# Optimization experiments

Hardware: AMD Instinct MI355X
Metric: run time of the kernel (lower is better)

The kernel has to match this reference:

```python
import jax, jax.numpy as jnp
import numpy as np

B, L, H = 4, 1024, 1024
NH, HD = 16, 64
ND = NH * HD
ITERS = 4
U = 5  # MSA1 ring window size (hard-coded in source)


def _conv1x1(w, b, x):  # w [O,C], b [O], x [B,C,L] -> [B,O,L]  (Conv2d 1x1 == per-position linear)
    return jnp.einsum('oc,bcl->bol', w, x) + b[None, :, None]


def _layernorm(x, s, b, eps=1e-5):  # x [B,H,L]; LayerNorm over channel dim H
    mu = x.mean(1, keepdims=True)
    var = ((x - mu) ** 2).mean(1, keepdims=True)
    return (x - mu) / jnp.sqrt(var + eps) * s[None, :, None] + b[None, :, None]


def _msa1(x, ax, wq, bq, wk, bk, wv, bv, wo, bo):
    # x [B,H,L] normalized nodes; ax [B,H,2,L] (ring embedding + relay)
    b, h, l = x.shape
    q = _conv1x1(wq, bq, x).reshape(b, NH, HD, l)
    k = _conv1x1(wk, bk, x).reshape(b, NH, HD, l)
    v = _conv1x1(wv, bv, x).reshape(b, NH, HD, l)
    pad = U // 2
    kp = jnp.pad(k, ((0, 0), (0, 0), (0, 0), (pad, pad)))
    vp = jnp.pad(v, ((0, 0), (0, 0), (0, 0), (pad, pad)))
    # F.unfold with (U,1) kernel along L == stack of U shifted views
    kw = jnp.stack([kp[..., u:u + l] for u in range(U)], axis=3)  # [B,NH,HD,U,L]
    vw = jnp.stack([vp[..., u:u + l] for u in range(U)], axis=3)
    al = ax.shape[2]
    ak = (jnp.einsum('oc,bcal->boal', wk, ax) + bk[None, :, None, None]).reshape(b, NH, HD, al, l)
    av = (jnp.einsum('oc,bcal->boal', wv, ax) + bv[None, :, None, None]).reshape(b, NH, HD, al, l)
    kw = jnp.concatenate([kw, ak], axis=3)  # [B,NH,HD,U+2,L]
    vw = jnp.concatenate([vw, av], axis=3)
    scores = (q[:, :, :, None, :] * kw).sum(2) / np.sqrt(HD)  # [B,NH,U+2,L]
    alphas = jax.nn.softmax(scores, axis=2)
    att = (alphas[:, :, None, :, :] * vw).sum(3).reshape(b, ND, l)
    return _conv1x1(wo, bo, att)  # [B,H,L]


def _msa2(relay, y, smask, wq, bq, wk, bk, wo, bo):
    # relay [B,H]; y [B,H,L+1]; smask [B,L+1] True at padding
    b = relay.shape[0]
    q = (jnp.einsum('oc,bc->bo', wq, relay) + bq).reshape(b, NH, HD)
    k = _conv1x1(wk, bk, y).reshape(b, NH, HD, -1)
    pre = jnp.einsum('bnd,bndl->bnl', q, k) / np.sqrt(HD)
    pre = jnp.where(smask[:, None, :], -1e10, pre)
    alphas = jax.nn.softmax(pre, axis=-1)
    # NOTE: source has v = k (WV output unused) -- reproduced faithfully
    att = jnp.einsum('bnl,bndl->bnd', alphas, k).reshape(b, ND)
    return jnp.einsum('oc,bc->bo', wo, att) + bo  # [B,H]


def _star_forward(data, mask, ln_s, ln_b, rwq, rwq_b, rwk, rwk_b, rwv, rwv_b, rwo, rwo_b,
                  swq, swq_b, swk, swk_b, swo, swo_b):
    b, l, h = data.shape
    pad_mask = (mask == 0)  # True at padding positions
    smask = jnp.concatenate([jnp.zeros((b, 1), bool), pad_mask], axis=1)  # [B,L+1]
    embs = jnp.transpose(data, (0, 2, 1))  # [B,H,L]
    nodes = embs
    relay = embs.mean(2)  # [B,H]
    for i in range(ITERS):
        xn = _layernorm(nodes, ln_s[i], ln_b[i])
        ax = jnp.stack([embs, jnp.broadcast_to(relay[:, :, None], embs.shape)], axis=2)  # [B,H,2,L]
        ring = _msa1(xn, ax, rwq[i], rwq_b[i], rwk[i], rwk_b[i], rwv[i], rwv_b[i], rwo[i], rwo_b[i])
        nodes = nodes + jax.nn.leaky_relu(ring)
        y = jnp.concatenate([relay[:, :, None], nodes], axis=2)  # [B,H,L+1]
        relay = jax.nn.leaky_relu(_msa2(relay, y, smask, swq[i], swq_b[i], swk[i], swk_b[i], swo[i], swo_b[i]))
        nodes = jnp.where(pad_mask[:, None, :], 0.0, nodes)
    return jnp.transpose(nodes, (0, 2, 1)), relay  # [B,L,H], [B,H]


def setup_inputs() -> dict:
    key = jax.random.key(0)
    ks = jax.random.split(key, 16)
    def p(k, shape):
        return jax.random.normal(k, shape, jnp.float32) * 0.02
    return dict(
        data=jax.random.normal(ks[0], (B, L, H), jnp.float32),
        mask=jax.random.randint(ks[1], (B, L), 0, 2).astype(jnp.int32),
        ln_s=jnp.ones((ITERS, H), jnp.float32),
        ln_b=jnp.zeros((ITERS, H), jnp.float32),
        rwq=p(ks[2], (ITERS, ND, H)), rwq_b=p(ks[3], (ITERS, ND)),
        rwk=p(ks[4], (ITERS, ND, H)), rwk_b=p(ks[5], (ITERS, ND)),
        rwv=p(ks[6], (ITERS, ND, H)), rwv_b=p(ks[7], (ITERS, ND)),
        rwo=p(ks[8], (ITERS, H, ND)), rwo_b=p(ks[9], (ITERS, H)),
        swq=p(ks[10], (ITERS, ND, H)), swq_b=p(ks[11], (ITERS, ND)),
        swk=p(ks[12], (ITERS, ND, H)), swk_b=p(ks[13], (ITERS, ND)),
        swo=p(ks[14], (ITERS, H, ND)), swo_b=p(ks[15], (ITERS, H)),
    )


def reference(data, mask, ln_s, ln_b, rwq, rwq_b, rwk, rwk_b, rwv, rwv_b, rwo, rwo_b,
              swq, swq_b, swk, swk_b, swo, swo_b):
    return _star_forward(data, mask, ln_s, ln_b, rwq, rwq_b, rwk, rwk_b, rwv, rwv_b,
                         rwo, rwo_b, swq, swq_b, swk, swk_b, swo, swo_b)
```

## Files before the change

kernel.cpp:

```cpp
#include <hip/hip_runtime.h>
#include <math.h>

namespace {

constexpr int B_ = 4, L_ = 1024, H_ = 1024, NH_ = 16, HD_ = 64, ND_ = 1024, ITERS_ = 4;

typedef unsigned short u16;
typedef __attribute__((ext_vector_type(8))) short short8;
typedef __attribute__((ext_vector_type(4))) float f32x4;

__device__ inline u16 f2bf(float f) {
  unsigned u = __builtin_bit_cast(unsigned, f);
  u += 0x7FFFu + ((u >> 16) & 1u);
  return (u16)(u >> 16);
}
__device__ inline float bf2f(u16 v) {
  unsigned u = ((unsigned)v) << 16;
  return __builtin_bit_cast(float, u);
}

__device__ inline void gl_lds16(const u16* g, u16* l) {
  __builtin_amdgcn_global_load_lds((const __attribute__((address_space(1))) void*)g,
                                   (__attribute__((address_space(3))) void*)l, 16, 0, 0);
}

__global__ void k_prep(const float* __restrict__ data, const float* __restrict__ rwq,
                       const float* __restrict__ rwk, const float* __restrict__ rwv,
                       const float* __restrict__ rwo, const float* __restrict__ swk,
                       u16* __restrict__ embs_bf, u16* __restrict__ wq_bf,
                       u16* __restrict__ wk_bf, u16* __restrict__ wv_bf,
                       u16* __restrict__ wo_bf, u16* __restrict__ swk_bf,
                       float* __restrict__ nodes) {
  int i = blockIdx.x * 256 + threadIdx.x;
  int which = blockIdx.y;
  if (which == 6) {
    reinterpret_cast<float4*>(nodes)[i] = reinterpret_cast<const float4*>(data)[i];
    return;
  }
  const float* src;
  u16* dst;
  switch (which) {
    case 0: src = data; dst = embs_bf; break;
    case 1: src = rwq; dst = wq_bf; break;
    case 2: src = rwk; dst = wk_bf; break;
    case 3: src = rwv; dst = wv_bf; break;
    case 4: src = rwo; dst = wo_bf; break;
    default: src = swk; dst = swk_bf; break;
  }
  float4 v = reinterpret_cast<const float4*>(src)[i];
  ushort4 o;
  o.x = f2bf(v.x); o.y = f2bf(v.y); o.z = f2bf(v.z); o.w = f2bf(v.w);
  reinterpret_cast<ushort4*>(dst)[i] = o;
}

__global__ void k_relay_part(const float* __restrict__ data, float* __restrict__ part) {
  int b = blockIdx.z, chunk = blockIdx.y;
  int c = blockIdx.x * 256 + threadIdx.x;
  const float* p = data + ((size_t)b * L_ + chunk * 128) * H_ + c;
  float acc = 0.f;
  for (int l = 0; l < 128; ++l) acc += p[(size_t)l * H_];
  part[((size_t)b * 8 + chunk) * H_ + c] = acc;
}
__global__ void k_relay_reduce(const float* __restrict__ part, float* __restrict__ relay) {
  int i = blockIdx.x * 256 + threadIdx.x;
  int b = i >> 10, c = i & 1023;
  float acc = 0.f;
  for (int j = 0; j < 8; ++j) acc += part[((size_t)b * 8 + j) * H_ + c];
  relay[i] = acc * (1.f / (float)L_);
}

__global__ __launch_bounds__(256) void k_layernorm_bf(float* __restrict__ nodes,
                                                      const float* __restrict__ s,
                                                      const float* __restrict__ bb,
                                                      const int* __restrict__ mask,
                                                      u16* __restrict__ y, int do_zero) {
  int row = blockIdx.x * 4 + (threadIdx.x >> 6);
  int lane = threadIdx.x & 63;
  int b = row >> 10, l = row & 1023;
  bool pad = do_zero && (mask[b * L_ + l] == 0);
  float4* xr = reinterpret_cast<float4*>(nodes + (size_t)row * H_);
  float4 v[4];
  float sum = 0.f, sq = 0.f;
#pragma unroll
  for (int j = 0; j < 4; ++j) {
    v[j] = pad ? float4{0.f, 0.f, 0.f, 0.f} : xr[lane + 64 * j];
    sum += v[j].x + v[j].y + v[j].z + v[j].w;
    sq += v[j].x * v[j].x + v[j].y * v[j].y + v[j].z * v[j].z + v[j].w * v[j].w;
  }
  if (pad) {
#pragma unroll
    for (int j = 0; j < 4; ++j) xr[lane + 64 * j] = float4{0.f, 0.f, 0.f, 0.f};
  }
#pragma unroll
  for (int off = 32; off; off >>= 1) {
    sum += __shfl_xor(sum, off);
    sq += __shfl_xor(sq, off);
  }
  float mu = sum * (1.f / (float)H_);
  float rstd = rsqrtf(sq * (1.f / (float)H_) - mu * mu + 1e-5f);
  ushort4* yr = reinterpret_cast<ushort4*>(y + (size_t)row * H_);
#pragma unroll
  for (int j = 0; j < 4; ++j) {
    int c4 = lane + 64 * j;
    float4 sc = reinterpret_cast<const float4*>(s)[c4];
    float4 bc = reinterpret_cast<const float4*>(bb)[c4];
    ushort4 o;
    o.x = f2bf((v[j].x - mu) * rstd * sc.x + bc.x);
    o.y = f2bf((v[j].y - mu) * rstd * sc.y + bc.y);
    o.z = f2bf((v[j].z - mu) * rstd * sc.z + bc.z);
    o.w = f2bf((v[j].w - mu) * rstd * sc.w + bc.w);
    yr[c4] = o;
  }
}


#define GEMM_PROLOGUE(XPTR, WPTR)                                              \
  __shared__ __align__(16) u16 sX[2][128 * 32];                                \
  __shared__ __align__(16) u16 sW[2][128 * 32];                                \
  const int t = threadIdx.x;                                                   \
  const int w = t >> 6, lane = t & 63;                                         \
  const int wm = w >> 1, wn = w & 1;                                           \
  const int r4 = lane >> 2, slot = lane & 3;                                   \
  const int rowS0 = w * 16 + r4, rowS1 = 64 + rowS0;                           \
  const int colS0 = ((slot ^ ((rowS0 >> 1) & 3)) << 3);                        \
  const int colS1 = ((slot ^ ((rowS1 >> 1) & 3)) << 3);                        \
  const u16* gX0 = (XPTR) + (size_t)(bm + rowS0) * 1024 + colS0;               \
  const u16* gX1 = (XPTR) + (size_t)(bm + rowS1) * 1024 + colS1;               \
  const u16* gW0 = (WPTR) + (size_t)(bn + rowS0) * 1024 + colS0;               \
  const u16* gW1 = (WPTR) + (size_t)(bn + rowS1) * 1024 + colS1;               \
  u16* lX0a = sX[0] + w * 512;                                                 \
  u16* lX0b = sX[1] + w * 512;                                                 \
  u16* lX1a = sX[0] + (4 + w) * 512;                                           \
  u16* lX1b = sX[1] + (4 + w) * 512;                                           \
  u16* lW0a = sW[0] + w * 512;                                                 \
  u16* lW0b = sW[1] + w * 512;                                                 \
  u16* lW1a = sW[0] + (4 + w) * 512;                                           \
  u16* lW1b = sW[1] + (4 + w) * 512;                                           \
  const int kidx = (((lane >> 4) ^ ((lane >> 1) & 3)) << 3);                   \
  f32x4 acc[4][4];                                                             \
  _Pragma("unroll") for (int i_ = 0; i_ < 4; ++i_)                             \
      _Pragma("unroll") for (int j_ = 0; j_ < 4; ++j_)                         \
          acc[i_][j_] = f32x4{0.f, 0.f, 0.f, 0.f};

#define GEMM_KLOOP64(AROWBASE, BROWBASE, ASRC, BSRC)                           \
  for (int ck = 0; ck < 1024; ck += 64) {                                      \
    gl_lds16(gX0, lX0a);                                                       \
    gl_lds16(gX0 + 32, lX0b);                                                  \
    gl_lds16(gX1, lX1a);                                                       \
    gl_lds16(gX1 + 32, lX1b);                                                  \
    gl_lds16(gW0, lW0a);                                                       \
    gl_lds16(gW0 + 32, lW0b);                                                  \
    gl_lds16(gW1, lW1a);                                                       \
    gl_lds16(gW1 + 32, lW1b);                                                  \
    gX0 += 64; gX1 += 64; gW0 += 64; gW1 += 64;                                \
    __syncthreads();                                                           \
    _Pragma("unroll") for (int h = 0; h < 2; ++h) {                            \
      short8 af_[4], bf_[4];                                                   \
      _Pragma("unroll") for (int mf = 0; mf < 4; ++mf)                         \
          af_[mf] = *reinterpret_cast<const short8*>(                          \
              &ASRC[h][((AROWBASE) + mf * 16) * 32 + kidx]);                   \
      _Pragma("unroll") for (int nf = 0; nf < 4; ++nf)                         \
          bf_[nf] = *reinterpret_cast<const short8*>(                          \
              &BSRC[h][((BROWBASE) + nf * 16) * 32 + kidx]);                   \
      _Pragma("unroll") for (int mf = 0; mf < 4; ++mf)                         \
          _Pragma("unroll") for (int nf = 0; nf < 4; ++nf)                     \
              acc[mf][nf] = __builtin_amdgcn_mfma_f32_16x16x32_bf16(           \
                  af_[mf], bf_[nf], acc[mf][nf], 0, 0, 0);                     \
    }                                                                          \
    __syncthreads();                                                          \
  }

__global__ __launch_bounds__(256, 3) void k_gemm5(const u16* __restrict__ wq,
                                                  const u16* __restrict__ wk,
                                                  const u16* __restrict__ wv,
                                                  const float* __restrict__ bq,
                                                  const float* __restrict__ bk,
                                                  const float* __restrict__ bv,
                                                  const u16* __restrict__ xn,
                                                  const u16* __restrict__ embs,
                                                  u16* __restrict__ Y) {
  const int orig = blockIdx.y * 32 + blockIdx.x;
  const int swz = (orig & 7) * 160 + (orig >> 3);
  const int sbx = swz & 31, sby = swz >> 5;
  const int bm = sbx * 128;
  const int which = sby >> 3;
  const int bn = (sby & 7) * 128;
  const u16* W = (which == 0) ? wq : ((which == 1 || which == 3) ? wk : wv);
  const float* bias = (which == 0) ? bq : ((which == 1 || which == 3) ? bk : bv);
  const u16* X = (which < 3) ? xn : embs;
  u16* Yw = Y + (size_t)which * ((size_t)B_ * L_ * ND_);

  GEMM_PROLOGUE(X, W)
  const int rW = wm * 64 + (lane & 15);
  const int rX = wn * 64 + (lane & 15);
  GEMM_KLOOP64(rW, rX, sW, sX)

#pragma unroll
  for (int mo = 0; mo < 4; ++mo) {
    int o0 = bn + wm * 64 + mo * 16 + ((lane >> 4) << 2);
    float4 bs = *reinterpret_cast<const float4*>(bias + o0);
#pragma unroll
    for (int nl = 0; nl < 4; ++nl) {
      int bl = bm + wn * 64 + nl * 16 + (lane & 15);
      f32x4 vv = acc[mo][nl];
      ushort4 ov;
      ov.x = f2bf(vv[0] + bs.x);
      ov.y = f2bf(vv[1] + bs.y);
      ov.z = f2bf(vv[2] + bs.z);
      ov.w = f2bf(vv[3] + bs.w);
      *reinterpret_cast<ushort4*>(&Yw[(size_t)bl * 1024 + o0]) = ov;
    }
  }
}

__global__ __launch_bounds__(256, 3) void k_gemm_wo(const u16* __restrict__ W,
                                                    const float* __restrict__ bias,
                                                    const u16* __restrict__ X,
                                                    float* __restrict__ nodes,
                                                    u16* __restrict__ nodes_bf) {
  const int orig = blockIdx.y * 32 + blockIdx.x;
  const int swz = (orig & 7) * 32 + (orig >> 3);
  const int bm = (swz & 31) * 128;
  const int bn = (swz >> 5) * 128;
  GEMM_PROLOGUE(X, W)
  const int rW = wm * 64 + (lane & 15);
  const int rX = wn * 64 + (lane & 15);
  GEMM_KLOOP64(rW, rX, sW, sX)

#pragma unroll
  for (int mo = 0; mo < 4; ++mo) {
    int o0 = bn + wm * 64 + mo * 16 + ((lane >> 4) << 2);
    float4 bs = *reinterpret_cast<const float4*>(bias + o0);
#pragma unroll
    for (int nl = 0; nl < 4; ++nl) {
      int bl = bm + wn * 64 + nl * 16 + (lane & 15);
      size_t ni = (size_t)bl * 1024 + o0;
      float4 curv = *reinterpret_cast<const float4*>(&nodes[ni]);
      f32x4 vv = acc[mo][nl];
      float r0 = vv[0] + bs.x; r0 = curv.x + (r0 > 0.f ? r0 : 0.01f * r0);
      float r1 = vv[1] + bs.y; r1 = curv.y + (r1 > 0.f ? r1 : 0.01f * r1);
      float r2 = vv[2] + bs.z; r2 = curv.z + (r2 > 0.f ? r2 : 0.01f * r2);
      float r3 = vv[3] + bs.w; r3 = curv.w + (r3 > 0.f ? r3 : 0.01f * r3);
      *reinterpret_cast<float4*>(&nodes[ni]) = float4{r0, r1, r2, r3};
      ushort4 ov;
      ov.x = f2bf(r0); ov.y = f2bf(r1); ov.z = f2bf(r2); ov.w = f2bf(r3);
      *reinterpret_cast<ushort4*>(&nodes_bf[ni]) = ov;
    }
  }
}

__global__ __launch_bounds__(256, 3) void k_gemm_kkb(const u16* __restrict__ W,
                                                     const float* __restrict__ bias,
                                                     const u16* __restrict__ X,
                                                     float* __restrict__ Y) {
  const int orig = blockIdx.y * 32 + blockIdx.x;
  const int swz = (orig & 7) * 32 + (orig >> 3);
  const int bm = (swz & 31) * 128;
  const int bn = (swz >> 5) * 128;
  GEMM_PROLOGUE(X, W)
  const int rX = wm * 64 + (lane & 15);
  const int rW = wn * 64 + (lane & 15);
  GEMM_KLOOP64(rX, rW, sX, sW)

#pragma unroll
  for (int nf = 0; nf < 4; ++nf) {
    int o = bn + wn * 64 + nf * 16 + (lane & 15);
    float bs = bias[o];
#pragma unroll
    for (int mf = 0; mf < 4; ++mf) {
      int gl = bm + wm * 64 + mf * 16 + ((lane >> 4) << 2);
      int b = gl >> 10, l = gl & 1023;
      size_t yi = ((size_t)(b * 1024 + o)) * (size_t)(L_ + 1) + 1 + l;
      f32x4 v = acc[mf][nf];
#pragma unroll
      for (int r = 0; r < 4; ++r) Y[yi + r] = v[r] + bs;
    }
  }
}

__global__ __launch_bounds__(256) void k_matvec2(const float* __restrict__ W0,
                                                 const float* __restrict__ b0,
                                                 float* __restrict__ y0, long sB0, long sO0,
                                                 const float* __restrict__ W1,
                                                 const float* __restrict__ b1,
                                                 float* __restrict__ y1, long sB1, long sO1,
                                                 const float* __restrict__ x) {
  int b = blockIdx.y;
  int z = blockIdx.z;
  const float* W = z ? W1 : W0;
  const float* bias = z ? b1 : b0;
  float* y = z ? y1 : y0;
  long sB = z ? sB1 : sB0, sO = z ? sO1 : sO0;
  int o = blockIdx.x * 4 + (threadIdx.x >> 6);
  int lane = threadIdx.x & 63;
  const float* wr = W + (size_t)o * 1024;
  const float* xb = x + (size_t)b * 1024;
  float acc = 0.f;
  for (int c = lane; c < 1024; c += 64) acc += wr[c] * xb[c];
#pragma unroll
  for (int off = 32; off; off >>= 1) acc += __shfl_xor(acc, off);
  if (lane == 0) y[(size_t)b * sB + (size_t)o * sO] = acc + bias[o];
}

__global__ __launch_bounds__(256) void k_matvec(const float* __restrict__ W,
                                                const float* __restrict__ bias,
                                                const float* __restrict__ x,
                                                float* __restrict__ y, int leaky) {
  int b = blockIdx.y;
  int o = blockIdx.x * 4 + (threadIdx.x >> 6);
  int lane = threadIdx.x & 63;
  const float* wr = W + (size_t)o * 1024;
  const float* xb = x + (size_t)b * 1024;
  float acc = 0.f;
  for (int c = lane; c < 1024; c += 64) acc += wr[c] * xb[c];
#pragma unroll
  for (int off = 32; off; off >>= 1) acc += __shfl_xor(acc, off);
  if (lane == 0) {
    acc += bias[o];
    if (leaky) acc = acc > 0.f ? acc : 0.01f * acc;
    y[(size_t)b * 1024 + o] = acc;
  }
}

__global__ __launch_bounds__(256) void k_msa1(const u16* __restrict__ q,
                                              const u16* __restrict__ k,
                                              const u16* __restrict__ v,
                                              const u16* __restrict__ ke,
                                              const u16* __restrict__ ve,
                                              const float* __restrict__ rk,
                                              const float* __restrict__ rv,
                                              u16* __restrict__ attbf) {
  int t = threadIdx.x;
  int wv = t >> 6, lane = t & 63;
  int head = lane >> 2, dq = lane & 3;
  int l = blockIdx.x * 4 + wv;
  int b = blockIdx.z;
  size_t row = ((size_t)(b * 1024 + l)) * 1024 + head * 64 + dq * 16;
  size_t rbase = (size_t)b * 1024 + head * 64 + dq * 16;

  float qf[16];
  {
    const short8* qp = reinterpret_cast<const short8*>(q + row);
#pragma unroll
    for (int j = 0; j < 2; ++j) {
      short8 qv = qp[j];
#pragma unroll
      for (int e = 0; e < 8; ++e) qf[j * 8 + e] = bf2f((u16)qv[e]);
    }
  }
  float s[7];
#pragma unroll
  for (int u = 0; u < 5; ++u) {
    int lk = l + u - 2;
    float su = 0.f;
    if (lk >= 0 && lk < L_) {
      const short8* kp = reinterpret_cast<const short8*>(
          k + ((size_t)(b * 1024 + lk)) * 1024 + head * 64 + dq * 16);
#pragma unroll
      for (int j = 0; j < 2; ++j) {
        short8 kv = kp[j];
#pragma unroll
        for (int e = 0; e < 8; ++e) su = fmaf(qf[j * 8 + e], bf2f((u16)kv[e]), su);
      }
    }
    s[u] = su;
  }
  {
    float su = 0.f;
    const short8* kp = reinterpret_cast<const short8*>(ke + row);
#pragma unroll
    for (int j = 0; j < 2; ++j) {
      short8 kv = kp[j];
#pragma unroll
      for (int e = 0; e < 8; ++e) su = fmaf(qf[j * 8 + e], bf2f((u16)kv[e]), su);
    }
    s[5] = su;
  }
  {
    float su = 0.f;
    const float4* rp = reinterpret_cast<const float4*>(rk + rbase);
#pragma unroll
    for (int j = 0; j < 4; ++j) {
      float4 r4 = rp[j];
      su = fmaf(qf[j * 4 + 0], r4.x, su);
      su = fmaf(qf[j * 4 + 1], r4.y, su);
      su = fmaf(qf[j * 4 + 2], r4.z, su);
      su = fmaf(qf[j * 4 + 3], r4.w, su);
    }
    s[6] = su;
  }
#pragma unroll
  for (int u = 0; u < 7; ++u) {
    s[u] += __shfl_xor(s[u], 1);
    s[u] += __shfl_xor(s[u], 2);
  }
  float m = -1e30f;
#pragma unroll
  for (int u = 0; u < 7; ++u) {
    s[u] *= 0.125f;
    m = fmaxf(m, s[u]);
  }
  float e[7], tot = 0.f;
#pragma unroll
  for (int u = 0; u < 7; ++u) {
    e[u] = expf(s[u] - m);
    tot += e[u];
  }
  float inv = 1.f / tot;
#pragma unroll
  for (int u = 0; u < 7; ++u) e[u] *= inv;

  float av[16];
  {
    const float4* rp = reinterpret_cast<const float4*>(rv + rbase);
#pragma unroll
    for (int j = 0; j < 4; ++j) {
      float4 r4 = rp[j];
      av[j * 4 + 0] = e[6] * r4.x;
      av[j * 4 + 1] = e[6] * r4.y;
      av[j * 4 + 2] = e[6] * r4.z;
      av[j * 4 + 3] = e[6] * r4.w;
    }
  }
  {
    const short8* vp = reinterpret_cast<const short8*>(ve + row);
#pragma unroll
    for (int j = 0; j < 2; ++j) {
      short8 vvv = vp[j];
#pragma unroll
      for (int ee = 0; ee < 8; ++ee) av[j * 8 + ee] = fmaf(e[5], bf2f((u16)vvv[ee]), av[j * 8 + ee]);
    }
  }
#pragma unroll
  for (int u = 0; u < 5; ++u) {
    int lk = l + u - 2;
    if (lk >= 0 && lk < L_) {
      const short8* vp = reinterpret_cast<const short8*>(
          v + ((size_t)(b * 1024 + lk)) * 1024 + head * 64 + dq * 16);
#pragma unroll
      for (int j = 0; j < 2; ++j) {
        short8 vvv = vp[j];
#pragma unroll
        for (int ee = 0; ee < 8; ++ee) av[j * 8 + ee] = fmaf(e[u], bf2f((u16)vvv[ee]), av[j * 8 + ee]);
      }
    }
  }
  u16 ob[16];
#pragma unroll
  for (int j = 0; j < 16; ++j) ob[j] = f2bf(av[j]);
  uint4* d4 = reinterpret_cast<uint4*>(attbf + row);
  const uint4* s4 = reinterpret_cast<const uint4*>(ob);
  d4[0] = s4[0];
  d4[1] = s4[1];
}

__global__ __launch_bounds__(256) void k_msa2p(const float* __restrict__ rq,
                                               const float* __restrict__ kk,
                                               const int* __restrict__ mask,
                                               float* __restrict__ pw,
                                               float* __restrict__ pE) {
  int n = blockIdx.x, c = blockIdx.y, b = blockIdx.z;
  int tid = threadIdx.x;
  __shared__ float sq_[HD_];
  __shared__ float se[260];
  size_t rb = (size_t)(b * NH_ + n) * HD_;
  if (tid < HD_) sq_[tid] = rq[rb + tid];
  __syncthreads();
  const float* kb = kk + rb * (size_t)(L_ + 1);
  int p0 = c * 256;
  {
    int p = p0 + tid;
    float e;
    if (p > 0 && mask[b * L_ + p - 1] == 0) {
      e = 0.f;
    } else {
      float acc = 0.f;
      for (int d = 0; d < HD_; ++d) acc = fmaf(sq_[d], kb[(size_t)d * (L_ + 1) + p], acc);
      e = expf(acc * 0.125f);
    }
    se[tid] = e;
  }
  int nP = 256;
  if (c == 3) {
    nP = 257;
    if (tid == 0) {
      float e;
      if (mask[b * L_ + 1023] == 0) {
        e = 0.f;
      } else {
        float acc = 0.f;
        for (int d = 0; d < HD_; ++d) acc = fmaf(sq_[d], kb[(size_t)d * (L_ + 1) + 1024], acc);
        e = expf(acc * 0.125f);
      }
      se[256] = e;
    }
  }
  __syncthreads();
  int lane = tid & 63, w = tid >> 6;
  if (w == 0) {
    float E = 0.f;
    for (int i = lane; i < nP; i += 64) E += se[i];
#pragma unroll
    for (int off = 32; off; off >>= 1) E += __shfl_xor(E, off);
    if (lane == 0) pE[((size_t)(b * NH_ + n)) * 4 + c] = E;
  }
  for (int dd = 0; dd < 16; ++dd) {
    int d = w * 16 + dd;
    const float* kd = kb + (size_t)d * (L_ + 1) + p0;
    float a = 0.f;
    for (int i = lane; i < nP; i += 64) a = fmaf(se[i], kd[i], a);
#pragma unroll
    for (int off = 32; off; off >>= 1) a += __shfl_xor(a, off);
    if (lane == 0) pw[(((size_t)(b * NH_ + n)) * 4 + c) * HD_ + d] = a;
  }
}

__global__ void k_msa2r(const float* __restrict__ pw, const float* __restrict__ pE,
                        float* __restrict__ satt) {
  int i = blockIdx.x * 256 + threadIdx.x;
  int bn = i >> 6, d = i & 63;
  float E = pE[bn * 4 + 0] + pE[bn * 4 + 1] + pE[bn * 4 + 2] + pE[bn * 4 + 3];
  float ws = pw[((size_t)bn * 4 + 0) * HD_ + d] + pw[((size_t)bn * 4 + 1) * HD_ + d] +
             pw[((size_t)bn * 4 + 2) * HD_ + d] + pw[((size_t)bn * 4 + 3) * HD_ + d];
  satt[i] = ws / E;
}

__global__ void k_final(const float* __restrict__ nodes, const int* __restrict__ mask,
                        float* __restrict__ out) {
  int i = blockIdx.x * 256 + threadIdx.x;
  int row = i >> 8;
  int b = row >> 10, l = row & 1023;
  float4 v = (mask[b * L_ + l] == 0) ? float4{0.f, 0.f, 0.f, 0.f}
                                     : reinterpret_cast<const float4*>(nodes)[i];
  reinterpret_cast<float4*>(out)[i] = v;
}

__global__ void k_copy_relay(const float* __restrict__ relay, float* __restrict__ out) {
  int i = blockIdx.x * 256 + threadIdx.x;
  out[i] = relay[i];
}

}

extern "C" void kernel_launch(void* const* d_in, const int* in_sizes, int n_in,
                              void* d_out, int out_size, void* d_ws, size_t ws_size,
                              hipStream_t stream) {
  (void)in_sizes; (void)n_in; (void)out_size; (void)ws_size;
  const float* data = (const float*)d_in[0];
  const int* mask = (const int*)d_in[1];
  const float* ln_s = (const float*)d_in[2];
  const float* ln_b = (const float*)d_in[3];
  const float* rwq = (const float*)d_in[4];
  const float* rwq_b = (const float*)d_in[5];
  const float* rwk = (const float*)d_in[6];
  const float* rwk_b = (const float*)d_in[7];
  const float* rwv = (const float*)d_in[8];
  const float* rwv_b = (const float*)d_in[9];
  const float* rwo = (const float*)d_in[10];
  const float* rwo_b = (const float*)d_in[11];
  const float* swq = (const float*)d_in[12];
  const float* swq_b = (const float*)d_in[13];
  const float* swk = (const float*)d_in[14];
  const float* swk_b = (const float*)d_in[15];
  const float* swo = (const float*)d_in[16];
  const float* swo_b = (const float*)d_in[17];
  float* out = (float*)d_out;

  const size_t SZ = (size_t)B_ * ND_ * L_;
  float* f = (float*)d_ws;
  float* nodes = f; f += SZ;
  float* kkb = f; f += (size_t)B_ * ND_ * (L_ + 1);
  float* part = f; f += (size_t)B_ * 8 * H_;
  float* relay = f; f += B_ * H_;
  float* rk = f; f += B_ * ND_;
  float* rv = f; f += B_ * ND_;
  float* rq = f; f += B_ * ND_;
  float* satt = f; f += B_ * ND_;
  float* pw = f; f += (size_t)B_ * NH_ * 4 * HD_;
  float* pE = f; f += B_ * NH_ * 4;
  u16* u = (u16*)f;
  u16* xn_bf = u; u += SZ;
  u16* embs_bf = u; u += SZ;
  u16* att_bf = u; u += SZ;
  u16* nodes_bf = u; u += SZ;
  u16* qkv5_bf = u; u += 5 * SZ;
  u16* wq_bf = u; u += SZ;
  u16* wk_bf = u; u += SZ;
  u16* wv_bf = u; u += SZ;
  u16* wo_bf = u; u += SZ;
  u16* swk_bf = u; u += SZ;

  k_prep<<<dim3(4096, 7), 256, 0, stream>>>(data, rwq, rwk, rwv, rwo, swk,
                                            embs_bf, wq_bf, wk_bf, wv_bf, wo_bf, swk_bf, nodes);
  k_relay_part<<<dim3(H_ / 256, 8, B_), 256, 0, stream>>>(data, part);
  k_relay_reduce<<<dim3((B_ * H_) / 256), 256, 0, stream>>>(part, relay);

  for (int i = 0; i < ITERS_; ++i) {
    const u16* wq_i = wq_bf + (size_t)i * ND_ * H_;
    const u16* wk_i = wk_bf + (size_t)i * ND_ * H_;
    const u16* wv_i = wv_bf + (size_t)i * ND_ * H_;
    const u16* wo_i = wo_bf + (size_t)i * H_ * ND_;
    const u16* sk_i = swk_bf + (size_t)i * ND_ * H_;

    k_layernorm_bf<<<dim3(B_ * L_ / 4), 256, 0, stream>>>(nodes, ln_s + i * H_, ln_b + i * H_,
                                                          mask, xn_bf, i > 0 ? 1 : 0);
    k_gemm5<<<dim3(32, 40), 256, 0, stream>>>(wq_i, wk_i, wv_i,
                                              rwq_b + i * ND_, rwk_b + i * ND_, rwv_b + i * ND_,
                                              xn_bf, embs_bf, qkv5_bf);
    k_matvec2<<<dim3(256, B_, 2), 256, 0, stream>>>(
        rwk + (size_t)i * ND_ * H_, rwk_b + i * ND_, rk, ND_, 1,
        rwv + (size_t)i * ND_ * H_, rwv_b + i * ND_, rv, ND_, 1, relay);
    k_msa1<<<dim3(L_ / 4, 1, B_), 256, 0, stream>>>(qkv5_bf, qkv5_bf + SZ, qkv5_bf + 2 * SZ,
                                                    qkv5_bf + 3 * SZ, qkv5_bf + 4 * SZ, rk, rv, att_bf);
    k_gemm_wo<<<dim3(32, 8), 256, 0, stream>>>(wo_i, rwo_b + i * H_, att_bf, nodes, nodes_bf);
    k_matvec2<<<dim3(256, B_, 2), 256, 0, stream>>>(
        swq + (size_t)i * ND_ * H_, swq_b + i * ND_, rq, ND_, 1,
        swk + (size_t)i * ND_ * H_, swk_b + i * ND_, kkb, (long)ND_ * (L_ + 1), L_ + 1, relay);
    k_gemm_kkb<<<dim3(32, 8), 256, 0, stream>>>(sk_i, swk_b + i * ND_, nodes_bf, kkb);
    k_msa2p<<<dim3(NH_, 4, B_), 256, 0, stream>>>(rq, kkb, mask, pw, pE);
    k_msa2r<<<dim3((B_ * NH_ * HD_) / 256), 256, 0, stream>>>(pw, pE, satt);
    k_matvec<<<dim3(256, B_), 256, 0, stream>>>(swo + (size_t)i * H_ * ND_, swo_b + i * H_,
                                                satt, relay, 1);
  }
  k_final<<<4096, 256, 0, stream>>>(nodes, mask, out);
  k_copy_relay<<<dim3((B_ * H_) / 256), 256, 0, stream>>>(relay, out + (size_t)B_ * L_ * H_);
}
```

Before: 711.7 us.

## Merge relay matvecs, fuse msa2 reduce with swo, and shrink small GEMM tiles

The four relay matvecs (rk, rv, rq, and the kkb column 0) now run as one launch issued before gemm5, since they all depend only on the relay vector. The msa2 partial reduction is fused with the swo matvec so satt is kept in shared memory. The wo and kkb GEMMs use 128x64 tiles, giving 512 blocks instead of 256 for better CU fill. The block-index swizzle in gemm5 is removed. Together these cut launch count, expose more parallelism, and drop an intermediate buffer, at the risk of worse L2 locality without the swizzle. The fused msa2r_swo kernel also recomputes satt redundantly in every block.

```diff
diff --git a/kernel.cpp b/kernel.cpp
--- a/kernel.cpp
+++ b/kernel.cpp
@@ -179,12 +179,9 @@
                                                   const u16* __restrict__ xn,
                                                   const u16* __restrict__ embs,
                                                   u16* __restrict__ Y) {
-  const int orig = blockIdx.y * 32 + blockIdx.x;
-  const int swz = (orig & 7) * 160 + (orig >> 3);
-  const int sbx = swz & 31, sby = swz >> 5;
-  const int bm = sbx * 128;
-  const int which = sby >> 3;
-  const int bn = (sby & 7) * 128;
+  const int bm = blockIdx.x * 128;
+  const int which = blockIdx.y >> 3;
+  const int bn = (blockIdx.y & 7) * 128;
   const u16* W = (which == 0) ? wq : ((which == 1 || which == 3) ? wk : wv);
   const float* bias = (which == 0) ? bq : ((which == 1 || which == 3) ? bk : bv);
   const u16* X = (which < 3) ? xn : embs;
@@ -213,23 +210,74 @@
   }
 }
 
-__global__ __launch_bounds__(256, 3) void k_gemm_wo(const u16* __restrict__ W,
-                                                    const float* __restrict__ bias,
-                                                    const u16* __restrict__ X,
-                                                    float* __restrict__ nodes,
-                                                    u16* __restrict__ nodes_bf) {
-  const int orig = blockIdx.y * 32 + blockIdx.x;
-  const int swz = (orig & 7) * 32 + (orig >> 3);
-  const int bm = (swz & 31) * 128;
-  const int bn = (swz >> 5) * 128;
-  GEMM_PROLOGUE(X, W)
-  const int rW = wm * 64 + (lane & 15);
+
+#define SMALL_PROLOGUE(XPTR, WPTR)                                             \
+  __shared__ __align__(16) u16 sX[2][128 * 32];                                \
+  __shared__ __align__(16) u16 sW[2][64 * 32];                                 \
+  const int t = threadIdx.x;                                                   \
+  const int w = t >> 6, lane = t & 63;                                         \
+  const int wm = w >> 1, wn = w & 1;                                           \
+  const int r4 = lane >> 2, slot = lane & 3;                                   \
+  const int rowS0 = w * 16 + r4, rowS1 = 64 + rowS0;                           \
+  const int colS0 = ((slot ^ ((rowS0 >> 1) & 3)) << 3);                        \
+  const int colS1 = ((slot ^ ((rowS1 >> 1) & 3)) << 3);                        \
+  const u16* gX0 = (XPTR) + (size_t)(bm + rowS0) * 1024 + colS0;               \
+  const u16* gX1 = (XPTR) + (size_t)(bm + rowS1) * 1024 + colS1;               \
+  const u16* gW0 = (WPTR) + (size_t)(bn + rowS0) * 1024 + colS0;               \
+  u16* lX0a = sX[0] + w * 512;                                                 \
+  u16* lX0b = sX[1] + w * 512;                                                 \
+  u16* lX1a = sX[0] + (4 + w) * 512;                                           \
+  u16* lX1b = sX[1] + (4 + w) * 512;                                           \
+  u16* lW0a = sW[0] + w * 512;                                                 \
+  u16* lW0b = sW[1] + w * 512;                                                 \
+  const int kidx = (((lane >> 4) ^ ((lane >> 1) & 3)) << 3);
+
+#define SMALL_KLOOP(MFN, NFN, ACC, AROWBASE, BROWBASE, ASRC, BSRC)             \
+  for (int ck = 0; ck < 1024; ck += 64) {                                      \
+    gl_lds16(gX0, lX0a);                                                       \
+    gl_lds16(gX0 + 32, lX0b);                                                  \
+    gl_lds16(gX1, lX1a);                                                       \
+    gl_lds16(gX1 + 32, lX1b);                                                  \
+    gl_lds16(gW0, lW0a);                                                       \
+    gl_lds16(gW0 + 32, lW0b);                                                  \
+    gX0 += 64; gX1 += 64; gW0 += 64;                                           \
+    __syncthreads();                                                           \
+    _Pragma("unroll") for (int h = 0; h < 2; ++h) {                            \
+      short8 af_[MFN], bf_[NFN];                                               \
+      _Pragma("unroll") for (int mf = 0; mf < MFN; ++mf)                       \
+          af_[mf] = *reinterpret_cast<const short8*>(                          \
+              &ASRC[h][((AROWBASE) + mf * 16) * 32 + kidx]);                   \
+      _Pragma("unroll") for (int nf = 0; nf < NFN; ++nf)                       \
+          bf_[nf] = *reinterpret_cast<const short8*>(                          \
+              &BSRC[h][((BROWBASE) + nf * 16) * 32 + kidx]);                   \
+      _Pragma("unroll") for (int mf = 0; mf < MFN; ++mf)                       \
+          _Pragma("unroll") for (int nf = 0; nf < NFN; ++nf)                   \
+              ACC[mf][nf] = __builtin_amdgcn_mfma_f32_16x16x32_bf16(           \
+                  af_[mf], bf_[nf], ACC[mf][nf], 0, 0, 0);                     \
+    }                                                                          \
+    __syncthreads();                                                          \
+  }
+
+__global__ __launch_bounds__(256, 2) void k_gemm_wo_s(const u16* __restrict__ W,
+                                                      const float* __restrict__ bias,
+                                                      const u16* __restrict__ X,
+                                                      float* __restrict__ nodes,
+                                                      u16* __restrict__ nodes_bf) {
+  const int bm = blockIdx.x * 128;
+  const int bn = blockIdx.y * 64;
+  SMALL_PROLOGUE(X, W)
+  f32x4 acc[2][4];
+#pragma unroll
+  for (int i_ = 0; i_ < 2; ++i_)
+#pragma unroll
+    for (int j_ = 0; j_ < 4; ++j_) acc[i_][j_] = f32x4{0.f, 0.f, 0.f, 0.f};
+  const int rW = wm * 32 + (lane & 15);
   const int rX = wn * 64 + (lane & 15);
-  GEMM_KLOOP64(rW, rX, sW, sX)
-
-#pragma unroll
-  for (int mo = 0; mo < 4; ++mo) {
-    int o0 = bn + wm * 64 + mo * 16 + ((lane >> 4) << 2);
+  SMALL_KLOOP(2, 4, acc, rW, rX, sW, sX)
+
+#pragma unroll
+  for (int mo = 0; mo < 2; ++mo) {
+    int o0 = bn + wm * 32 + mo * 16 + ((lane >> 4) << 2);
     float4 bs = *reinterpret_cast<const float4*>(bias + o0);
 #pragma unroll
     for (int nl = 0; nl < 4; ++nl) {
@@ -249,22 +297,25 @@
   }
 }
 
-__global__ __launch_bounds__(256, 3) void k_gemm_kkb(const u16* __restrict__ W,
-                                                     const float* __restrict__ bias,
-                                                     const u16* __restrict__ X,
-                                                     float* __restrict__ Y) {
-  const int orig = blockIdx.y * 32 + blockIdx.x;
-  const int swz = (orig & 7) * 32 + (orig >> 3);
-  const int bm = (swz & 31) * 128;
-  const int bn = (swz >> 5) * 128;
-  GEMM_PROLOGUE(X, W)
+__global__ __launch_bounds__(256, 2) void k_gemm_kkb_s(const u16* __restrict__ W,
+                                                       const float* __restrict__ bias,
+                                                       const u16* __restrict__ X,
+                                                       float* __restrict__ Y) {
+  const int bm = blockIdx.x * 128;
+  const int bn = blockIdx.y * 64;
+  SMALL_PROLOGUE(X, W)
+  f32x4 acc[4][2];
+#pragma unroll
+  for (int i_ = 0; i_ < 4; ++i_)
+#pragma unroll
+    for (int j_ = 0; j_ < 2; ++j_) acc[i_][j_] = f32x4{0.f, 0.f, 0.f, 0.f};
   const int rX = wm * 64 + (lane & 15);
-  const int rW = wn * 64 + (lane & 15);
-  GEMM_KLOOP64(rX, rW, sX, sW)
-
-#pragma unroll
-  for (int nf = 0; nf < 4; ++nf) {
-    int o = bn + wn * 64 + nf * 16 + (lane & 15);
+  const int rW = wn * 32 + (lane & 15);
+  SMALL_KLOOP(4, 2, acc, rX, rW, sX, sW)
+
+#pragma unroll
+  for (int nf = 0; nf < 2; ++nf) {
+    int o = bn + wn * 32 + nf * 16 + (lane & 15);
     float bs = bias[o];
 #pragma unroll
     for (int mf = 0; mf < 4; ++mf) {
@@ -278,19 +329,19 @@
   }
 }
 
-__global__ __launch_bounds__(256) void k_matvec2(const float* __restrict__ W0,
-                                                 const float* __restrict__ b0,
-                                                 float* __restrict__ y0, long sB0, long sO0,
+__global__ __launch_bounds__(256) void k_matvec4(const float* __restrict__ W0,
+                                                 const float* __restrict__ b0, float* __restrict__ y0,
                                                  const float* __restrict__ W1,
-                                                 const float* __restrict__ b1,
-                                                 float* __restrict__ y1, long sB1, long sO1,
+                                                 const float* __restrict__ b1, float* __restrict__ y1,
+                                                 const float* __restrict__ W2,
+                                                 const float* __restrict__ b2, float* __restrict__ y2,
+                                                 const float* __restrict__ W3,
+                                                 const float* __restrict__ b3, float* __restrict__ y3,
+                                                 long sB3, long sO3,
                                                  const float* __restrict__ x) {
-  int b = blockIdx.y;
-  int z = blockIdx.z;
-  const float* W = z ? W1 : W0;
-  const float* bias = z ? b1 : b0;
-  float* y = z ? y1 : y0;
-  long sB = z ? sB1 : sB0, sO = z ? sO1 : sO0;
+  int b = blockIdx.y, z = blockIdx.z;
+  const float* W = (z == 0) ? W0 : (z == 1) ? W1 : (z == 2) ? W2 : W3;
+  const float* bias = (z == 0) ? b0 : (z == 1) ? b1 : (z == 2) ? b2 : b3;
   int o = blockIdx.x * 4 + (threadIdx.x >> 6);
   int lane = threadIdx.x & 63;
   const float* wr = W + (size_t)o * 1024;
@@ -299,26 +350,12 @@
   for (int c = lane; c < 1024; c += 64) acc += wr[c] * xb[c];
 #pragma unroll
   for (int off = 32; off; off >>= 1) acc += __shfl_xor(acc, off);
-  if (lane == 0) y[(size_t)b * sB + (size_t)o * sO] = acc + bias[o];
-}
-
-__global__ __launch_bounds__(256) void k_matvec(const float* __restrict__ W,
-                                                const float* __restrict__ bias,
-                                                const float* __restrict__ x,
-                                                float* __restrict__ y, int leaky) {
-  int b = blockIdx.y;
-  int o = blockIdx.x * 4 + (threadIdx.x >> 6);
-  int lane = threadIdx.x & 63;
-  const float* wr = W + (size_t)o * 1024;
-  const float* xb = x + (size_t)b * 1024;
-  float acc = 0.f;
-  for (int c = lane; c < 1024; c += 64) acc += wr[c] * xb[c];
-#pragma unroll
-  for (int off = 32; off; off >>= 1) acc += __shfl_xor(acc, off);
   if (lane == 0) {
     acc += bias[o];
-    if (leaky) acc = acc > 0.f ? acc : 0.01f * acc;
-    y[(size_t)b * 1024 + o] = acc;
+    if (z == 3) y3[(size_t)b * sB3 + (size_t)o * sO3] = acc;
+    else if (z == 2) y2[(size_t)b * 1024 + o] = acc;
+    else if (z == 1) y1[(size_t)b * 1024 + o] = acc;
+    else y0[(size_t)b * 1024 + o] = acc;
   }
 }
 
@@ -515,14 +552,35 @@
   }
 }
 
-__global__ void k_msa2r(const float* __restrict__ pw, const float* __restrict__ pE,
-                        float* __restrict__ satt) {
-  int i = blockIdx.x * 256 + threadIdx.x;
-  int bn = i >> 6, d = i & 63;
-  float E = pE[bn * 4 + 0] + pE[bn * 4 + 1] + pE[bn * 4 + 2] + pE[bn * 4 + 3];
-  float ws = pw[((size_t)bn * 4 + 0) * HD_ + d] + pw[((size_t)bn * 4 + 1) * HD_ + d] +
-             pw[((size_t)bn * 4 + 2) * HD_ + d] + pw[((size_t)bn * 4 + 3) * HD_ + d];
-  satt[i] = ws / E;
+__global__ __launch_bounds__(256) void k_msa2r_swo(const float* __restrict__ pw,
+                                                   const float* __restrict__ pE,
+                                                   const float* __restrict__ swo,
+                                                   const float* __restrict__ swo_b,
+                                                   float* __restrict__ relay) {
+  int b = blockIdx.y;
+  int tid = threadIdx.x;
+  __shared__ float satt[1024];
+#pragma unroll
+  for (int j = 0; j < 4; ++j) {
+    int idx = tid * 4 + j;
+    int bn = b * 16 + (idx >> 6), d = idx & 63;
+    float E = pE[bn * 4 + 0] + pE[bn * 4 + 1] + pE[bn * 4 + 2] + pE[bn * 4 + 3];
+    float ws = pw[((size_t)bn * 4 + 0) * HD_ + d] + pw[((size_t)bn * 4 + 1) * HD_ + d] +
+               pw[((size_t)bn * 4 + 2) * HD_ + d] + pw[((size_t)bn * 4 + 3) * HD_ + d];
+    satt[idx] = ws / E;
+  }
+  __syncthreads();
+  int o = blockIdx.x * 4 + (tid >> 6);
+  int lane = tid & 63;
+  const float* wr = swo + (size_t)o * 1024;
+  float acc = 0.f;
+  for (int c = lane; c < 1024; c += 64) acc = fmaf(wr[c], satt[c], acc);
+#pragma unroll
+  for (int off = 32; off; off >>= 1) acc += __shfl_xor(acc, off);
+  if (lane == 0) {
+    acc += swo_b[o];
+    relay[(size_t)b * 1024 + o] = acc > 0.f ? acc : 0.01f * acc;
+  }
 }
 
 __global__ void k_final(const float* __restrict__ nodes, const int* __restrict__ mask,
@@ -575,7 +633,6 @@
   float* rk = f; f += B_ * ND_;
   float* rv = f; f += B_ * ND_;
   float* rq = f; f += B_ * ND_;
-  float* satt = f; f += B_ * ND_;
   float* pw = f; f += (size_t)B_ * NH_ * 4 * HD_;
   float* pE = f; f += B_ * NH_ * 4;
   u16* u = (u16*)f;
@@ -604,23 +661,22 @@
 
     k_layernorm_bf<<<dim3(B_ * L_ / 4), 256, 0, stream>>>(nodes, ln_s + i * H_, ln_b + i * H_,
                                                           mask, xn_bf, i > 0 ? 1 : 0);
+    k_matvec4<<<dim3(256, B_, 4), 256, 0, stream>>>(
+        rwk + (size_t)i * ND_ * H_, rwk_b + i * ND_, rk,
+        rwv + (size_t)i * ND_ * H_, rwv_b + i * ND_, rv,
+        swq + (size_t)i * ND_ * H_, swq_b + i * ND_, rq,
+        swk + (size_t)i * ND_ * H_, swk_b + i * ND_, kkb, (long)ND_ * (L_ + 1), L_ + 1,
+        relay);
     k_gemm5<<<dim3(32, 40), 256, 0, stream>>>(wq_i, wk_i, wv_i,
                                               rwq_b + i * ND_, rwk_b + i * ND_, rwv_b + i * ND_,
                                               xn_bf, embs_bf, qkv5_bf);
-    k_matvec2<<<dim3(256, B_, 2), 256, 0, stream>>>(
-        rwk + (size_t)i * ND_ * H_, rwk_b + i * ND_, rk, ND_, 1,
-        rwv + (size_t)i * ND_ * H_, rwv_b + i * ND_, rv, ND_, 1, relay);
     k_msa1<<<dim3(L_ / 4, 1, B_), 256, 0, stream>>>(qkv5_bf, qkv5_bf + SZ, qkv5_bf + 2 * SZ,
                                                     qkv5_bf + 3 * SZ, qkv5_bf + 4 * SZ, rk, rv, att_bf);
-    k_gemm_wo<<<dim3(32, 8), 256, 0, stream>>>(wo_i, rwo_b + i * H_, att_bf, nodes, nodes_bf);
-    k_matvec2<<<dim3(256, B_, 2), 256, 0, stream>>>(
-        swq + (size_t)i * ND_ * H_, swq_b + i * ND_, rq, ND_, 1,
-        swk + (size_t)i * ND_ * H_, swk_b + i * ND_, kkb, (long)ND_ * (L_ + 1), L_ + 1, relay);
-    k_gemm_kkb<<<dim3(32, 8), 256, 0, stream>>>(sk_i, swk_b + i * ND_, nodes_bf, kkb);
+    k_gemm_wo_s<<<dim3(32, 16), 256, 0, stream>>>(wo_i, rwo_b + i * H_, att_bf, nodes, nodes_bf);
+    k_gemm_kkb_s<<<dim3(32, 16), 256, 0, stream>>>(sk_i, swk_b + i * ND_, nodes_bf, kkb);
     k_msa2p<<<dim3(NH_, 4, B_), 256, 0, stream>>>(rq, kkb, mask, pw, pE);
-    k_msa2r<<<dim3((B_ * NH_ * HD_) / 256), 256, 0, stream>>>(pw, pE, satt);
-    k_matvec<<<dim3(256, B_), 256, 0, stream>>>(swo + (size_t)i * H_ * ND_, swo_b + i * H_,
-                                                satt, relay, 1);
+    k_msa2r_swo<<<dim3(256, B_), 256, 0, stream>>>(pw, pE, swo + (size_t)i * H_ * ND_,
+                                                   swo_b + i * H_, relay);
   }
   k_final<<<4096, 256, 0, stream>>>(nodes, mask, out);
   k_copy_relay<<<dim3((B_ * H_) / 256), 256, 0, stream>>>(relay, out + (size_t)B_ * L_ * H_);
```

Result: faster. 631.9 us (-11.2%).
